# Performance work log

Hardware: AMD Instinct MI355X
Metric: run time of the kernel (lower is better)

Reference implementation:

```python
import jax, jax.numpy as jnp
import numpy as np

N_NODES = 20000
N_EDGES = 320000
NEG_SLOPE = 0.2


def gat_conv(x, src, dst, W, a_src, a_dst, b, concat):
    # x: [N, Fin]; W: [Fin, H*C]; a_src/a_dst: [H, C]; b: [H*C] or [C]
    N = x.shape[0]
    H, C = a_src.shape
    h = (x @ W).reshape(N, H, C)                      # [N, H, C]
    al_s = jnp.einsum('nhc,hc->nh', h, a_src)         # [N, H]
    al_d = jnp.einsum('nhc,hc->nh', h, a_dst)         # [N, H]
    e = jax.nn.leaky_relu(al_s[src] + al_d[dst], NEG_SLOPE)  # [E, H]
    # segment softmax over incoming edges of each dst node
    m = jax.ops.segment_max(e, dst, num_segments=N)   # [N, H]
    ex = jnp.exp(e - m[dst])
    denom = jax.ops.segment_sum(ex, dst, num_segments=N)
    alpha = ex / denom[dst]                           # [E, H]
    msg = alpha[:, :, None] * h[src]                  # [E, H, C]
    out = jax.ops.segment_sum(msg, dst, num_segments=N)  # [N, H, C]
    if concat:
        return out.reshape(N, H * C) + b
    return out.mean(axis=1) + b


def setup_inputs() -> dict:
    key = jax.random.key(0)
    ks = jax.random.split(key, 16)
    def g(k, shape, scale=0.05):
        return jax.random.normal(k, shape, dtype=jnp.float32) * scale
    x = jax.random.normal(ks[0], (N_NODES, 768), dtype=jnp.float32)
    edge_index = jax.random.randint(ks[1], (2, N_EDGES), 0, N_NODES, dtype=jnp.int32)
    return {
        'x': x, 'edge_index': edge_index,
        'W1': g(ks[2], (768, 1024)), 'a1_src': g(ks[3], (4, 256)), 'a1_dst': g(ks[4], (4, 256)), 'b1': g(ks[5], (1024,)),
        'W2': g(ks[6], (1024, 512)), 'a2_src': g(ks[7], (4, 128)), 'a2_dst': g(ks[8], (4, 128)), 'b2': g(ks[9], (512,)),
        'W3': g(ks[10], (512, 64)), 'a3_src': g(ks[11], (1, 64)), 'a3_dst': g(ks[12], (1, 64)), 'b3': g(ks[13], (64,)),
    }


def reference(x, edge_index, W1, a1_src, a1_dst, b1, W2, a2_src, a2_dst, b2, W3, a3_src, a3_dst, b3):
    N = x.shape[0]
    loops = jnp.arange(N, dtype=edge_index.dtype)
    src = jnp.concatenate([edge_index[0], loops])  # PyG GATConv adds self-loops
    dst = jnp.concatenate([edge_index[1], loops])
    h = gat_conv(x, src, dst, W1, a1_src, a1_dst, b1, concat=True)
    h = jax.nn.relu(h)
    h = gat_conv(h, src, dst, W2, a2_src, a2_dst, b2, concat=True)
    h = jax.nn.relu(h)
    h = gat_conv(h, src, dst, W3, a3_src, a3_dst, b3, concat=False)
    return jnp.tanh(h)
```

## Files before the change

kernel.cpp:

```cpp
#include <hip/hip_runtime.h>
#include <hip/hip_bf16.h>

#define NN 20000
#define NE 320000
#define ET 340000
#define NEG_SLOPE 0.2f

typedef __attribute__((ext_vector_type(8))) _Float16 f16x8;
typedef __attribute__((ext_vector_type(4))) _Float16 f16x4;
typedef __attribute__((ext_vector_type(4))) float f32x4;

typedef __attribute__((address_space(3))) unsigned int lds_u32_t;
typedef __attribute__((address_space(1))) unsigned int glb_u32_t;

__device__ __forceinline__ void gload_lds16(const void* g, void* l) {
  __builtin_amdgcn_global_load_lds((const glb_u32_t*)g, (lds_u32_t*)l, 16, 0, 0);
}

__global__ void k_zero(int* p, int n) {
  int i = blockIdx.x * blockDim.x + threadIdx.x;
  if (i < n) p[i] = 0;
}

__global__ void k_count(const int* __restrict__ ei, int* __restrict__ cnt) {
  int e = blockIdx.x * blockDim.x + threadIdx.x;
  if (e >= ET) return;
  int d = (e < NE) ? ei[NE + e] : (e - NE);
  atomicAdd(&cnt[d], 1);
}

__global__ __launch_bounds__(1024) void k_scan(const int* __restrict__ cnt,
                                               int* __restrict__ rptr,
                                               int* __restrict__ cursor) {
  const int CH = 20;
  int t = threadIdx.x, lane = t & 63, wid = t >> 6;
  int base = t * CH;
  int v[CH];
  int sum = 0;
#pragma unroll
  for (int j = 0; j < CH; ++j) {
    int idx = base + j;
    v[j] = (idx < NN) ? cnt[idx] : 0;
    sum += v[j];
  }
  int ws = sum;
#pragma unroll
  for (int off = 1; off < 64; off <<= 1) {
    int u = __shfl_up(ws, off);
    if (lane >= off) ws += u;
  }
  __shared__ int wsum[16];
  __shared__ int wpre[16];
  if (lane == 63) wsum[wid] = ws;
  __syncthreads();
  if (t == 0) {
    int acc = 0;
#pragma unroll
    for (int w = 0; w < 16; ++w) { wpre[w] = acc; acc += wsum[w]; }
  }
  __syncthreads();
  int run = wpre[wid] + ws - sum;
  if (t == 0) rptr[0] = 0;
#pragma unroll
  for (int j = 0; j < CH; ++j) {
    int idx = base + j;
    if (idx < NN) {
      cursor[idx] = run;
      run += v[j];
      rptr[idx + 1] = run;
    }
  }
}

__global__ void k_fill(const int* __restrict__ ei, int* __restrict__ cursor,
                       int* __restrict__ csrc, int* __restrict__ epos) {
  int e = blockIdx.x * blockDim.x + threadIdx.x;
  if (e >= ET) return;
  int s, d;
  if (e < NE) { s = ei[e]; d = ei[NE + e]; } else { s = d = e - NE; }
  int p = atomicAdd(&cursor[d], 1);
  csrc[p] = s;
  epos[e] = p;
}

__global__ void k_f2h4(const float* __restrict__ x, _Float16* __restrict__ o, int n4) {
  int i = blockIdx.x * blockDim.x + threadIdx.x;
  if (i >= n4) return;
  f32x4 v = *(const f32x4*)&x[i * 4];
  f16x4 h = { (_Float16)v.x, (_Float16)v.y, (_Float16)v.z, (_Float16)v.w };
  *(f16x4*)&o[i * 4] = h;
}

__global__ __launch_bounds__(256) void k_wt(const float* __restrict__ W,
                                            _Float16* __restrict__ Wt, int K, int N) {
  __shared__ float tile[32][33];
  int bk = blockIdx.y * 32, bn = blockIdx.x * 32;
  int tx = threadIdx.x & 31, ty = threadIdx.x >> 5;
#pragma unroll
  for (int r = ty; r < 32; r += 8) {
    int k = bk + r, n = bn + tx;
    tile[r][tx] = (k < K && n < N) ? W[(size_t)k * N + n] : 0.f;
  }
  __syncthreads();
#pragma unroll
  for (int r = ty; r < 32; r += 8) {
    int n = bn + r, k = bk + tx;
    if (n < N && k < K) Wt[(size_t)n * K + k] = (_Float16)tile[tx][r];
  }
}

__global__ __launch_bounds__(256) void k_gemm(const _Float16* __restrict__ A,
                                              const _Float16* __restrict__ B,
                                              _Float16* __restrict__ C,
                                              int M, int N, int K, int gx) {
  const int nb = gridDim.x;
  const int q = nb >> 3, r = nb & 7;
  const int xcd = blockIdx.x & 7, kk = blockIdx.x >> 3;
  const int l = (xcd < r) ? (xcd * (q + 1) + kk) : (r * (q + 1) + (xcd - r) * q + kk);
  const int bx = l % gx, by = l / gx;

  __shared__ __align__(16) _Float16 Al[128 * 32];
  __shared__ __align__(16) _Float16 Bl[128 * 32];
  const int tid = threadIdx.x;
  const int wave = tid >> 6, lane = tid & 63;
  const int wm = wave >> 1, wn = wave & 1;
  const int m0 = by * 128, n0 = bx * 128;
  const int fr = lane & 15, fk = (lane >> 4) * 8;
  f32x4 acc[4][4] = {};

  for (int k0 = 0; k0 < K; k0 += 32) {
#pragma unroll
    for (int c = 0; c < 2; ++c) {
      int s = (wave * 2 + c) * 64 + lane;
      int row = s >> 2, col = (s & 3) * 8;
      int ra = m0 + row; if (ra > M - 1) ra = M - 1;
      int rb = n0 + row; if (rb > N - 1) rb = N - 1;
      gload_lds16(A + (size_t)ra * K + k0 + col, &Al[(size_t)(wave * 2 + c) * 512]);
      gload_lds16(B + (size_t)rb * K + k0 + col, &Bl[(size_t)(wave * 2 + c) * 512]);
    }
    __syncthreads();
    f16x8 af[4], bf[4];
#pragma unroll
    for (int i = 0; i < 4; ++i) {
      af[i] = *(const f16x8*)&Al[(wm * 64 + i * 16 + fr) * 32 + fk];
      bf[i] = *(const f16x8*)&Bl[(wn * 64 + i * 16 + fr) * 32 + fk];
    }
#pragma unroll
    for (int mi = 0; mi < 4; ++mi)
#pragma unroll
      for (int ni = 0; ni < 4; ++ni)
        acc[mi][ni] = __builtin_amdgcn_mfma_f32_16x16x32_f16(af[mi], bf[ni], acc[mi][ni], 0, 0, 0);
    __syncthreads();
  }

  const int r0 = (lane >> 4) * 4, cn = lane & 15;
#pragma unroll
  for (int mi = 0; mi < 4; ++mi)
#pragma unroll
    for (int ni = 0; ni < 4; ++ni) {
      int gm = m0 + wm * 64 + mi * 16 + r0;
      int gn = n0 + wn * 64 + ni * 16 + cn;
      if (gn < N) {
#pragma unroll
        for (int rr = 0; rr < 4; ++rr)
          if (gm + rr < M) C[(size_t)(gm + rr) * N + gn] = (_Float16)acc[mi][ni][rr];
      }
    }
}

__global__ void k_logits(const _Float16* __restrict__ h, const float* __restrict__ as_,
                         const float* __restrict__ ad_, float* __restrict__ als,
                         float* __restrict__ ald, int H, int C) {
  int pair = blockIdx.x * 4 + (threadIdx.x >> 6);
  if (pair >= NN * H) return;
  int lane = threadIdx.x & 63;
  int hd = pair % H;
  const _Float16* hp = h + (size_t)pair * C;
  float s = 0.f, d = 0.f;
  for (int c = lane * 4; c < C; c += 256) {
    f16x4 v = *(const f16x4*)&hp[c];
#pragma unroll
    for (int j = 0; j < 4; ++j) {
      float f = (float)v[j];
      s += f * as_[hd * C + c + j];
      d += f * ad_[hd * C + c + j];
    }
  }
#pragma unroll
  for (int off = 32; off; off >>= 1) {
    s += __shfl_down(s, off);
    d += __shfl_down(d, off);
  }
  if (lane == 0) { als[pair] = s; ald[pair] = d; }
}

template <int H>
__global__ void k_esoft(const int* __restrict__ ei, const float* __restrict__ als,
                        const float* __restrict__ ald, const int* __restrict__ epos,
                        float* __restrict__ den, float* __restrict__ ex) {
  int idx = blockIdx.x * blockDim.x + threadIdx.x;
  if (idx >= ET * H) return;
  int e = idx / H, hd = idx - e * H;
  int s, d;
  if (e < NE) { s = ei[e]; d = ei[NE + e]; } else { s = d = e - NE; }
  float v = als[s * H + hd] + ald[d * H + hd];
  v = v > 0.f ? v : NEG_SLOPE * v;
  float xv = __expf(v);
  ex[(size_t)epos[e] * H + hd] = xv;
  atomicAdd(&den[d * H + hd], xv);
}

template <int H, int C, int MODE>
__global__ __launch_bounds__(256) void k_aggw(
    const _Float16* __restrict__ h, const float* __restrict__ ex,
    const float* __restrict__ den, const int* __restrict__ rptr,
    const int* __restrict__ csrc, const float* __restrict__ bias,
    _Float16* __restrict__ oh, float* __restrict__ of) {
  constexpr int HC = H * C;
  constexpr int CPL = HC / 64;
  constexpr int NV = CPL / 8;
  const int wave = threadIdx.x >> 6, lane = threadIdx.x & 63;
  const int n = blockIdx.x * 4 + wave;
  const int c0 = lane * CPL;
  const int hd = c0 / C;
  const float invd = 1.f / den[n * H + hd];
  const int e0 = rptr[n], e1 = rptr[n + 1];
  float acc[CPL];
#pragma unroll
  for (int j = 0; j < CPL; ++j) acc[j] = 0.f;

  float xA = 0.f, xB = 0.f;
  f16x8 hA[NV], hB[NV];

#define LD_ROW(I, X, HV)                                                     \
  do {                                                                       \
    int _i = (I);                                                            \
    if (_i < e1) {                                                           \
      int _s = csrc[_i];                                                     \
      (X) = ex[(size_t)_i * H + hd] * invd;                                  \
      const _Float16* _hp = h + (size_t)_s * HC + c0;                        \
      _Pragma("unroll")                                                      \
      for (int _v = 0; _v < NV; ++_v) (HV)[_v] = *(const f16x8*)(_hp + _v * 8); \
    }                                                                        \
  } while (0)

  LD_ROW(e0, xA, hA);
  LD_ROW(e0 + 1, xB, hB);

  for (int i = e0; i < e1; i += 2) {
    {
      float a = xA;
      f16x8 t[NV];
#pragma unroll
      for (int v = 0; v < NV; ++v) t[v] = hA[v];
      LD_ROW(i + 2, xA, hA);
#pragma unroll
      for (int v = 0; v < NV; ++v)
#pragma unroll
        for (int j = 0; j < 8; ++j) acc[v * 8 + j] += a * (float)t[v][j];
    }
    if (i + 1 < e1) {
      float a = xB;
      f16x8 t[NV];
#pragma unroll
      for (int v = 0; v < NV; ++v) t[v] = hB[v];
      LD_ROW(i + 3, xB, hB);
#pragma unroll
      for (int v = 0; v < NV; ++v)
#pragma unroll
        for (int j = 0; j < 8; ++j) acc[v * 8 + j] += a * (float)t[v][j];
    }
  }
#undef LD_ROW

#pragma unroll
  for (int v = 0; v < NV; ++v) {
    f16x8 o;
#pragma unroll
    for (int j = 0; j < 8; ++j) {
      float r = acc[v * 8 + j] + bias[c0 + v * 8 + j];
      o[j] = (_Float16)(r > 0.f ? r : 0.f);
    }
    __builtin_nontemporal_store(o, (f16x8*)&oh[(size_t)n * HC + c0 + v * 8]);
  }
}

__global__ __launch_bounds__(64) void k_agg_last(
    const _Float16* __restrict__ h, const float* __restrict__ ex,
    const float* __restrict__ den, const int* __restrict__ rptr,
    const int* __restrict__ csrc, const float* __restrict__ bias,
    float* __restrict__ of) {
  int n = blockIdx.x;
  int t = threadIdx.x;
  float acc = 0.f;
  float invd = 1.f / den[n];
  int e0 = rptr[n], e1 = rptr[n + 1];
  for (int i = e0; i < e1; ++i) {
    int s = csrc[i];
    float a = ex[i];
    acc += a * (float)h[(size_t)s * 64 + t];
  }
  of[(size_t)n * 64 + t] = tanhf(acc * invd + bias[t]);
}

static inline size_t alup(size_t x) { return (x + 255) & ~(size_t)255; }

struct Scratch {
  _Float16* xb; _Float16* wtb; _Float16* h;
  float* als; float* ald; float* den; float* ex;
  int* cnt; int* rptr; int* cursor; int* csrc; int* epos;
};

static void run_layer(hipStream_t stream, const Scratch& S, const _Float16* xin,
                      int K, int N, int H, int C,
                      const float* W, const float* as_, const float* ad_, const float* bias,
                      int mode, const int* ei, _Float16* oh, float* of) {
  dim3 gt((N + 31) / 32, (K + 31) / 32);
  k_wt<<<gt, 256, 0, stream>>>(W, S.wtb, K, N);
  int gx = (N + 127) / 128, gy = (NN + 127) / 128;
  k_gemm<<<gx * gy, 256, 0, stream>>>(xin, S.wtb, S.h, NN, N, K, gx);
  k_logits<<<(NN * H + 3) / 4, 256, 0, stream>>>(S.h, as_, ad_, S.als, S.ald, H, C);
  k_zero<<<(NN * H + 255) / 256, 256, 0, stream>>>((int*)S.den, NN * H);
  if (H == 4) {
    k_esoft<4><<<(ET * 4 + 255) / 256, 256, 0, stream>>>(ei, S.als, S.ald, S.epos, S.den, S.ex);
  } else {
    k_esoft<1><<<(ET + 255) / 256, 256, 0, stream>>>(ei, S.als, S.ald, S.epos, S.den, S.ex);
  }
  if (mode == 0) {
    if (C == 256)      k_aggw<4, 256, 0><<<NN / 4, 256, 0, stream>>>(S.h, S.ex, S.den, S.rptr, S.csrc, bias, oh, of);
    else if (C == 128) k_aggw<4, 128, 0><<<NN / 4, 256, 0, stream>>>(S.h, S.ex, S.den, S.rptr, S.csrc, bias, oh, of);
  } else {
    k_agg_last<<<NN, 64, 0, stream>>>(S.h, S.ex, S.den, S.rptr, S.csrc, bias, of);
  }
}

extern "C" void kernel_launch(void* const* d_in, const int* in_sizes, int n_in,
                              void* d_out, int out_size, void* d_ws, size_t ws_size,
                              hipStream_t stream) {
  const float* x   = (const float*)d_in[0];
  const int*   ei  = (const int*)d_in[1];
  const float* W1  = (const float*)d_in[2];
  const float* a1s = (const float*)d_in[3];
  const float* a1d = (const float*)d_in[4];
  const float* b1  = (const float*)d_in[5];
  const float* W2  = (const float*)d_in[6];
  const float* a2s = (const float*)d_in[7];
  const float* a2d = (const float*)d_in[8];
  const float* b2  = (const float*)d_in[9];
  const float* W3  = (const float*)d_in[10];
  const float* a3s = (const float*)d_in[11];
  const float* a3d = (const float*)d_in[12];
  const float* b3  = (const float*)d_in[13];
  float* out = (float*)d_out;

  char* p = (char*)d_ws;
  Scratch S;
  S.xb  = (_Float16*)p; p += alup((size_t)NN * 1024 * 2);
  S.wtb = (_Float16*)p; p += alup((size_t)1024 * 1024 * 2);
  S.h   = (_Float16*)p; p += alup((size_t)NN * 1024 * 2);
  S.als = (float*)p;    p += alup((size_t)NN * 4 * 4);
  S.ald = (float*)p;    p += alup((size_t)NN * 4 * 4);
  S.den = (float*)p;    p += alup((size_t)NN * 4 * 4);
  S.ex  = (float*)p;    p += alup((size_t)ET * 4 * 4);
  S.cnt = (int*)p;      p += alup((size_t)NN * 4);
  S.rptr= (int*)p;      p += alup((size_t)(NN + 1) * 4);
  S.cursor=(int*)p;     p += alup((size_t)NN * 4);
  S.csrc= (int*)p;      p += alup((size_t)ET * 4);
  S.epos= (int*)p;      p += alup((size_t)ET * 4);

  k_zero<<<(NN + 255) / 256, 256, 0, stream>>>(S.cnt, NN);
  k_count<<<(ET + 255) / 256, 256, 0, stream>>>(ei, S.cnt);
  k_scan<<<1, 1024, 0, stream>>>(S.cnt, S.rptr, S.cursor);
  k_fill<<<(ET + 255) / 256, 256, 0, stream>>>(ei, S.cursor, S.csrc, S.epos);

  k_f2h4<<<(NN * 768 / 4 + 255) / 256, 256, 0, stream>>>(x, S.xb, NN * 768 / 4);

  run_layer(stream, S, S.xb, 768, 1024, 4, 256, W1, a1s, a1d, b1, 0, ei, S.xb, nullptr);
  run_layer(stream, S, S.xb, 1024, 512, 4, 128, W2, a2s, a2d, b2, 0, ei, S.xb, nullptr);
  run_layer(stream, S, S.xb, 512, 64, 1, 64, W3, a3s, a3d, b3, 1, ei, nullptr, out);
}
```

Baseline: 479.3 us.

## Fuse attention logits into GEMM epilogue and softmax into aggregation

The separate logits kernel is removed. Per-row attention dot products are now computed in the GEMM epilogue from the accumulators, with cross-lane shuffles and atomic adds into zeroed als/ald buffers. The edge-softmax kernel, with its ex/epos buffers and denominator atomics, is also removed: the aggregation kernels recompute leaky-relu and exp per edge and accumulate the denominator locally, normalizing at the end. This cuts several launches and the per-edge global traffic, at the cost of redundant exp work per lane, global atomics in the GEMM epilogue, and skipping the max subtraction, which was already absent before.

```diff
diff --git a/kernel.cpp b/kernel.cpp
--- a/kernel.cpp
+++ b/kernel.cpp
@@ -73,14 +73,13 @@
 }
 
 __global__ void k_fill(const int* __restrict__ ei, int* __restrict__ cursor,
-                       int* __restrict__ csrc, int* __restrict__ epos) {
+                       int* __restrict__ csrc) {
   int e = blockIdx.x * blockDim.x + threadIdx.x;
   if (e >= ET) return;
   int s, d;
   if (e < NE) { s = ei[e]; d = ei[NE + e]; } else { s = d = e - NE; }
   int p = atomicAdd(&cursor[d], 1);
   csrc[p] = s;
-  epos[e] = p;
 }
 
 __global__ void k_f2h4(const float* __restrict__ x, _Float16* __restrict__ o, int n4) {
@@ -112,7 +111,12 @@
 __global__ __launch_bounds__(256) void k_gemm(const _Float16* __restrict__ A,
                                               const _Float16* __restrict__ B,
                                               _Float16* __restrict__ C,
-                                              int M, int N, int K, int gx) {
+                                              const float* __restrict__ a_src,
+                                              const float* __restrict__ a_dst,
+                                              float* __restrict__ als,
+                                              float* __restrict__ ald,
+                                              int M, int N, int K, int gx,
+                                              int H, int Ch) {
   const int nb = gridDim.x;
   const int q = nb >> 3, r = nb & 7;
   const int xcd = blockIdx.x & 7, kk = blockIdx.x >> 3;
@@ -154,6 +158,7 @@
   }
 
   const int r0 = (lane >> 4) * 4, cn = lane & 15;
+
 #pragma unroll
   for (int mi = 0; mi < 4; ++mi)
 #pragma unroll
@@ -166,54 +171,51 @@
           if (gm + rr < M) C[(size_t)(gm + rr) * N + gn] = (_Float16)acc[mi][ni][rr];
       }
     }
-}
-
-__global__ void k_logits(const _Float16* __restrict__ h, const float* __restrict__ as_,
-                         const float* __restrict__ ad_, float* __restrict__ als,
-                         float* __restrict__ ald, int H, int C) {
-  int pair = blockIdx.x * 4 + (threadIdx.x >> 6);
-  if (pair >= NN * H) return;
-  int lane = threadIdx.x & 63;
-  int hd = pair % H;
-  const _Float16* hp = h + (size_t)pair * C;
-  float s = 0.f, d = 0.f;
-  for (int c = lane * 4; c < C; c += 256) {
-    f16x4 v = *(const f16x4*)&hp[c];
-#pragma unroll
-    for (int j = 0; j < 4; ++j) {
-      float f = (float)v[j];
-      s += f * as_[hd * C + c + j];
-      d += f * ad_[hd * C + c + j];
-    }
-  }
-#pragma unroll
-  for (int off = 32; off; off >>= 1) {
-    s += __shfl_down(s, off);
-    d += __shfl_down(d, off);
-  }
-  if (lane == 0) { als[pair] = s; ald[pair] = d; }
-}
-
-template <int H>
-__global__ void k_esoft(const int* __restrict__ ei, const float* __restrict__ als,
-                        const float* __restrict__ ald, const int* __restrict__ epos,
-                        float* __restrict__ den, float* __restrict__ ex) {
-  int idx = blockIdx.x * blockDim.x + threadIdx.x;
-  if (idx >= ET * H) return;
-  int e = idx / H, hd = idx - e * H;
-  int s, d;
-  if (e < NE) { s = ei[e]; d = ei[NE + e]; } else { s = d = e - NE; }
-  float v = als[s * H + hd] + ald[d * H + hd];
-  v = v > 0.f ? v : NEG_SLOPE * v;
-  float xv = __expf(v);
-  ex[(size_t)epos[e] * H + hd] = xv;
-  atomicAdd(&den[d * H + hd], xv);
+
+  const int colbase = n0 + wn * 64;
+  if (colbase < N) {
+    const int hd = colbase / Ch;
+    const int cin = colbase % Ch;
+    float asv[4], adv[4];
+#pragma unroll
+    for (int ni = 0; ni < 4; ++ni) {
+      int cc = colbase + ni * 16 + cn;
+      bool ok = cc < N;
+      int ci = hd * Ch + cin + ni * 16 + cn;
+      asv[ni] = ok ? a_src[ci] : 0.f;
+      adv[ni] = ok ? a_dst[ci] : 0.f;
+    }
+#pragma unroll
+    for (int mi = 0; mi < 4; ++mi) {
+#pragma unroll
+      for (int rr = 0; rr < 4; ++rr) {
+        float sv = 0.f, dv = 0.f;
+#pragma unroll
+        for (int ni = 0; ni < 4; ++ni) {
+          sv += acc[mi][ni][rr] * asv[ni];
+          dv += acc[mi][ni][rr] * adv[ni];
+        }
+#pragma unroll
+        for (int off = 1; off < 16; off <<= 1) {
+          sv += __shfl_xor(sv, off);
+          dv += __shfl_xor(dv, off);
+        }
+        if ((lane & 15) == 0) {
+          int gm = m0 + wm * 64 + mi * 16 + r0 + rr;
+          if (gm < M) {
+            atomicAdd(&als[gm * H + hd], sv);
+            atomicAdd(&ald[gm * H + hd], dv);
+          }
+        }
+      }
+    }
+  }
 }
 
 template <int H, int C, int MODE>
 __global__ __launch_bounds__(256) void k_aggw(
-    const _Float16* __restrict__ h, const float* __restrict__ ex,
-    const float* __restrict__ den, const int* __restrict__ rptr,
+    const _Float16* __restrict__ h, const float* __restrict__ als,
+    const float* __restrict__ ald, const int* __restrict__ rptr,
     const int* __restrict__ csrc, const float* __restrict__ bias,
     _Float16* __restrict__ oh, float* __restrict__ of) {
   constexpr int HC = H * C;
@@ -223,62 +225,70 @@
   const int n = blockIdx.x * 4 + wave;
   const int c0 = lane * CPL;
   const int hd = c0 / C;
-  const float invd = 1.f / den[n * H + hd];
+  const float aldn = ald[n * H + hd];
   const int e0 = rptr[n], e1 = rptr[n + 1];
   float acc[CPL];
 #pragma unroll
   for (int j = 0; j < CPL; ++j) acc[j] = 0.f;
-
-  float xA = 0.f, xB = 0.f;
+  float den = 0.f;
+
+  float lA = 0.f, lB = 0.f;
   f16x8 hA[NV], hB[NV];
 
-#define LD_ROW(I, X, HV)                                                     \
+#define LD_ROW(I, L, HV)                                                     \
   do {                                                                       \
     int _i = (I);                                                            \
     if (_i < e1) {                                                           \
       int _s = csrc[_i];                                                     \
-      (X) = ex[(size_t)_i * H + hd] * invd;                                  \
+      (L) = als[_s * H + hd];                                                \
       const _Float16* _hp = h + (size_t)_s * HC + c0;                        \
       _Pragma("unroll")                                                      \
       for (int _v = 0; _v < NV; ++_v) (HV)[_v] = *(const f16x8*)(_hp + _v * 8); \
     }                                                                        \
   } while (0)
 
-  LD_ROW(e0, xA, hA);
-  LD_ROW(e0 + 1, xB, hB);
+  LD_ROW(e0, lA, hA);
+  LD_ROW(e0 + 1, lB, hB);
 
   for (int i = e0; i < e1; i += 2) {
     {
-      float a = xA;
+      float v = lA + aldn;
       f16x8 t[NV];
 #pragma unroll
-      for (int v = 0; v < NV; ++v) t[v] = hA[v];
-      LD_ROW(i + 2, xA, hA);
-#pragma unroll
-      for (int v = 0; v < NV; ++v)
-#pragma unroll
-        for (int j = 0; j < 8; ++j) acc[v * 8 + j] += a * (float)t[v][j];
+      for (int vv = 0; vv < NV; ++vv) t[vv] = hA[vv];
+      LD_ROW(i + 2, lA, hA);
+      v = v > 0.f ? v : NEG_SLOPE * v;
+      float xv = __expf(v);
+      den += xv;
+#pragma unroll
+      for (int vv = 0; vv < NV; ++vv)
+#pragma unroll
+        for (int j = 0; j < 8; ++j) acc[vv * 8 + j] += xv * (float)t[vv][j];
     }
     if (i + 1 < e1) {
-      float a = xB;
+      float v = lB + aldn;
       f16x8 t[NV];
 #pragma unroll
-      for (int v = 0; v < NV; ++v) t[v] = hB[v];
-      LD_ROW(i + 3, xB, hB);
-#pragma unroll
-      for (int v = 0; v < NV; ++v)
-#pragma unroll
-        for (int j = 0; j < 8; ++j) acc[v * 8 + j] += a * (float)t[v][j];
+      for (int vv = 0; vv < NV; ++vv) t[vv] = hB[vv];
+      LD_ROW(i + 3, lB, hB);
+      v = v > 0.f ? v : NEG_SLOPE * v;
+      float xv = __expf(v);
+      den += xv;
+#pragma unroll
+      for (int vv = 0; vv < NV; ++vv)
+#pragma unroll
+        for (int j = 0; j < 8; ++j) acc[vv * 8 + j] += xv * (float)t[vv][j];
     }
   }
 #undef LD_ROW
 
+  float invd = 1.f / den;
 #pragma unroll
   for (int v = 0; v < NV; ++v) {
     f16x8 o;
 #pragma unroll
     for (int j = 0; j < 8; ++j) {
-      float r = acc[v * 8 + j] + bias[c0 + v * 8 + j];
+      float r = acc[v * 8 + j] * invd + bias[c0 + v * 8 + j];
       o[j] = (_Float16)(r > 0.f ? r : 0.f);
     }
     __builtin_nontemporal_store(o, (f16x8*)&oh[(size_t)n * HC + c0 + v * 8]);
@@ -286,51 +296,49 @@
 }
 
 __global__ __launch_bounds__(64) void k_agg_last(
-    const _Float16* __restrict__ h, const float* __restrict__ ex,
-    const float* __restrict__ den, const int* __restrict__ rptr,
+    const _Float16* __restrict__ h, const float* __restrict__ als,
+    const float* __restrict__ ald, const int* __restrict__ rptr,
     const int* __restrict__ csrc, const float* __restrict__ bias,
     float* __restrict__ of) {
   int n = blockIdx.x;
   int t = threadIdx.x;
-  float acc = 0.f;
-  float invd = 1.f / den[n];
+  float acc = 0.f, den = 0.f;
+  float aldn = ald[n];
   int e0 = rptr[n], e1 = rptr[n + 1];
   for (int i = e0; i < e1; ++i) {
     int s = csrc[i];
-    float a = ex[i];
-    acc += a * (float)h[(size_t)s * 64 + t];
-  }
-  of[(size_t)n * 64 + t] = tanhf(acc * invd + bias[t]);
+    float v = als[s] + aldn;
+    v = v > 0.f ? v : NEG_SLOPE * v;
+    float xv = __expf(v);
+    den += xv;
+    acc += xv * (float)h[(size_t)s * 64 + t];
+  }
+  of[(size_t)n * 64 + t] = tanhf(acc / den + bias[t]);
 }
 
 static inline size_t alup(size_t x) { return (x + 255) & ~(size_t)255; }
 
 struct Scratch {
   _Float16* xb; _Float16* wtb; _Float16* h;
-  float* als; float* ald; float* den; float* ex;
-  int* cnt; int* rptr; int* cursor; int* csrc; int* epos;
+  float* als; float* ald;
+  int* cnt; int* rptr; int* cursor; int* csrc;
 };
 
 static void run_layer(hipStream_t stream, const Scratch& S, const _Float16* xin,
                       int K, int N, int H, int C,
                       const float* W, const float* as_, const float* ad_, const float* bias,
-                      int mode, const int* ei, _Float16* oh, float* of) {
+                      int mode, _Float16* oh, float* of) {
   dim3 gt((N + 31) / 32, (K + 31) / 32);
   k_wt<<<gt, 256, 0, stream>>>(W, S.wtb, K, N);
+  k_zero<<<(2 * NN * H + 255) / 256, 256, 0, stream>>>((int*)S.als, 2 * NN * H);
   int gx = (N + 127) / 128, gy = (NN + 127) / 128;
-  k_gemm<<<gx * gy, 256, 0, stream>>>(xin, S.wtb, S.h, NN, N, K, gx);
-  k_logits<<<(NN * H + 3) / 4, 256, 0, stream>>>(S.h, as_, ad_, S.als, S.ald, H, C);
-  k_zero<<<(NN * H + 255) / 256, 256, 0, stream>>>((int*)S.den, NN * H);
-  if (H == 4) {
-    k_esoft<4><<<(ET * 4 + 255) / 256, 256, 0, stream>>>(ei, S.als, S.ald, S.epos, S.den, S.ex);
+  k_gemm<<<gx * gy, 256, 0, stream>>>(xin, S.wtb, S.h, as_, ad_, S.als, S.ald,
+                                      NN, N, K, gx, H, C);
+  if (mode == 0) {
+    if (C == 256)      k_aggw<4, 256, 0><<<NN / 4, 256, 0, stream>>>(S.h, S.als, S.ald, S.rptr, S.csrc, bias, oh, of);
+    else if (C == 128) k_aggw<4, 128, 0><<<NN / 4, 256, 0, stream>>>(S.h, S.als, S.ald, S.rptr, S.csrc, bias, oh, of);
   } else {
-    k_esoft<1><<<(ET + 255) / 256, 256, 0, stream>>>(ei, S.als, S.ald, S.epos, S.den, S.ex);
-  }
-  if (mode == 0) {
-    if (C == 256)      k_aggw<4, 256, 0><<<NN / 4, 256, 0, stream>>>(S.h, S.ex, S.den, S.rptr, S.csrc, bias, oh, of);
-    else if (C == 128) k_aggw<4, 128, 0><<<NN / 4, 256, 0, stream>>>(S.h, S.ex, S.den, S.rptr, S.csrc, bias, oh, of);
-  } else {
-    k_agg_last<<<NN, 64, 0, stream>>>(S.h, S.ex, S.den, S.rptr, S.csrc, bias, of);
+    k_agg_last<<<NN, 64, 0, stream>>>(S.h, S.als, S.ald, S.rptr, S.csrc, bias, of);
   }
 }
 
@@ -358,24 +366,25 @@
   S.xb  = (_Float16*)p; p += alup((size_t)NN * 1024 * 2);
   S.wtb = (_Float16*)p; p += alup((size_t)1024 * 1024 * 2);
   S.h   = (_Float16*)p; p += alup((size_t)NN * 1024 * 2);
-  S.als = (float*)p;    p += alup((size_t)NN * 4 * 4);
-  S.ald = (float*)p;    p += alup((size_t)NN * 4 * 4);
-  S.den = (float*)p;    p += alup((size_t)NN * 4 * 4);
-  S.ex  = (float*)p;    p += alup((size_t)ET * 4 * 4);
+  S.als = (float*)p;    p += alup((size_t)2 * NN * 4 * 4);
+  S.ald = S.als + NN * 4;
   S.cnt = (int*)p;      p += alup((size_t)NN * 4);
   S.rptr= (int*)p;      p += alup((size_t)(NN + 1) * 4);
   S.cursor=(int*)p;     p += alup((size_t)NN * 4);
   S.csrc= (int*)p;      p += alup((size_t)ET * 4);
-  S.epos= (int*)p;      p += alup((size_t)ET * 4);
+
 
   k_zero<<<(NN + 255) / 256, 256, 0, stream>>>(S.cnt, NN);
   k_count<<<(ET + 255) / 256, 256, 0, stream>>>(ei, S.cnt);
   k_scan<<<1, 1024, 0, stream>>>(S.cnt, S.rptr, S.cursor);
-  k_fill<<<(ET + 255) / 256, 256, 0, stream>>>(ei, S.cursor, S.csrc, S.epos);
+  k_fill<<<(ET + 255) / 256, 256, 0, stream>>>(ei, S.cursor, S.csrc);
 
   k_f2h4<<<(NN * 768 / 4 + 255) / 256, 256, 0, stream>>>(x, S.xb, NN * 768 / 4);
 
-  run_layer(stream, S, S.xb, 768, 1024, 4, 256, W1, a1s, a1d, b1, 0, ei, S.xb, nullptr);
-  run_layer(stream, S, S.xb, 1024, 512, 4, 128, W2, a2s, a2d, b2, 0, ei, S.xb, nullptr);
-  run_layer(stream, S, S.xb, 512, 64, 1, 64, W3, a3s, a3d, b3, 1, ei, nullptr, out);
-}
+  S.ald = S.als + NN * 4;
+  run_layer(stream, S, S.xb, 768, 1024, 4, 256, W1, a1s, a1d, b1, 0, S.xb, nullptr);
+  S.ald = S.als + NN * 4;
+  run_layer(stream, S, S.xb, 1024, 512, 4, 128, W2, a2s, a2d, b2, 0, S.xb, nullptr);
+  S.ald = S.als + NN * 1;
+  run_layer(stream, S, S.xb, 512, 64, 1, 64, W3, a3s, a3d, b3, 1, nullptr, out);
+}
```

New measurement: 441.1 us. -8.0%, faster.
